# Optimization experiments

Hardware: AMD Instinct MI355X
Metric: run time of the kernel (lower is better)

## Reference

```python
import jax, jax.numpy as jnp
import numpy as np

B_CAPS, C_CAPS, KSZ, STRIDE, N_ITER = 32, 32, 3, 2, 3


def setup_inputs() -> dict:
    key = jax.random.key(0)
    k1, k2, k3, k4, k5 = jax.random.split(key, 5)
    b, Bc, Cc, Win = 8, B_CAPS, C_CAPS, 13
    pose = 0.5 * jax.random.normal(k1, (b, 16 * Bc, Win, Win), jnp.float32)
    act = 0.05 + 0.9 * jax.random.uniform(k2, (b, Bc, Win, Win), jnp.float32)
    x = jnp.concatenate([pose, act], axis=1)
    W = 0.3 * jax.random.normal(k3, (KSZ, KSZ, Bc, Cc, 4, 4), jnp.float32)
    beta_v = jax.random.normal(k4, (1,), jnp.float32)
    beta_a = jax.random.normal(k5, (1,), jnp.float32)
    lambda_ = jnp.ones((1,), jnp.float32)
    return {"x": x, "W": W, "beta_v": beta_v, "beta_a": beta_a, "lambda_": lambda_}


def _conv_caps(x, W, beta_v, beta_a, lambda_):
    B, C, K, s, n_iter = B_CAPS, C_CAPS, KSZ, STRIDE, N_ITER
    b, Win = x.shape[0], x.shape[2]
    Wout = (Win - K) // s + 1
    # channel layout of pose is (4,4,B) row-major, per the original .view(-1,4,4,B,...)
    pose = x[:, :-B].reshape(b, 4, 4, B, Win, Win)
    act = x[:, -B:]
    ks = jnp.arange(K)
    Iidx = s * jnp.arange(Wout)[None, :] + ks[:, None]  # (K,Wout): i_in = s*x + ki
    Ir = Iidx[:, None, :, None]  # (K,1,Wout,1)
    Ic = Iidx[None, :, None, :]  # (1,K,1,Wout)
    # pose patches: (b,4,4,B,K,K,Wout,Wout); matrix dims are (q=rows, r=cols)
    pp = pose[:, :, :, :, Ir, Ic]
    # votes[n,o,ki,kj,x,y,c,p,r] = sum_q W[ki,kj,o,c,p,q] * pose[n,q,r,o,ki,kj,x,y]
    votes = jnp.einsum('ijocpq,nqroijxy->noijxycpr', W, pp)
    votes = votes.reshape(b, B, K, K, Wout, Wout, C, 16)
    a_patch = act[:, :, Ir, Ic]  # (b,B,K,K,Wout,Wout)
    # original E-step indexes votes at pos = stride*x - i, which is <=0 and wraps
    # (torch negative indexing) to (-ki) % K.  Faithfully reproduce that permutation.
    kperm = (-ks) % K
    votesE = votes[:, :, kperm][:, :, :, kperm]
    # routing weights kept in patch form R[i_in=s*x+ki, j_in=s*y+kj, x, y] -> (ki,kj,x,y);
    # this is exactly the set of R entries the original ever reads or writes.
    Rp = jnp.full((b, B, K, K, Wout, Wout, C), 1.0 / (Wout * Wout * C), x.dtype)
    TWO_PI = np.float32(2.0 * np.pi)
    lam = jnp.reshape(lambda_, ())
    mu = act_out = None
    for it in range(n_iter):
        # ---- M-step ----
        r_hat = Rp * a_patch[..., None]                      # (b,B,K,K,Wo,Wo,C)
        sum_r = r_hat.sum(axis=(1, 2, 3))                    # (b,Wo,Wo,C)
        mu = jnp.einsum('noijxyc,noijxycd->nxycd', r_hat, votes) / sum_r[..., None]
        mu_b = mu[:, None, None, None]                       # (b,1,1,1,Wo,Wo,C,16)
        sigma = jnp.einsum('noijxyc,noijxycd->nxycd', r_hat, (votes - mu_b) ** 2) / sum_r[..., None]
        cost = (beta_v + jnp.log(sigma)) * sum_r[..., None]  # (b,Wo,Wo,C,16)
        act_out = jax.nn.sigmoid(lam * (beta_a - cost.sum(-1)))  # (b,Wo,Wo,C)
        # ---- E-step (skipped on last iter: its R is never read afterwards) ----
        if it < n_iter - 1:
            # original: p = exp(-(V-mu)^2)/sqrt(2*pi*sigma), prod over 16 pose dims
            p = jnp.prod(jnp.exp(-(votesE - mu_b) ** 2) / jnp.sqrt(TWO_PI * sigma[:, None, None, None]), axis=-1)
            p_hat = act_out[:, None, None, None] * p         # (b,B,K,K,Wo,Wo,C)
            T = p_hat.sum(-1)                                # (b,B,K,K,Wo,Wo)
            # normalizer is per (batch, input-type, input-position): scatter-add over
            # all (ki,x),(kj,y) mapping to the same input pixel, summed over C
            D = jnp.zeros((b, B, Win, Win), x.dtype).at[:, :, Ir, Ic].add(T)
            Rp = p_hat / D[:, :, Ir, Ic][..., None]
    mus = mu.transpose(0, 3, 4, 1, 2).reshape(b, C * 16, Wout, Wout)
    acts = act_out.transpose(0, 3, 1, 2)                     # (b,C,Wo,Wo)
    return jnp.concatenate([mus, acts], axis=1)              # (b, C*17, Wo, Wo)


def reference(x, W, beta_v, beta_a, lambda_):
    return _conv_caps(x, W, beta_v, beta_a, lambda_)
```

## Files before the change

kernel.cpp:

```cpp
#include <hip/hip_runtime.h>


typedef float v2f __attribute__((ext_vector_type(2)));
typedef float v4f __attribute__((ext_vector_type(4)));

#define OFF_PHAT 0
#define OFF_D0   2654208
#define OFF_D1   2697472
#define OFF_POST 2740736
#define OFF_ACTT 3432960
#define OFF_WT2  3476224

__device__ __forceinline__ float wred64(float v) {
#pragma unroll
  for (int m = 32; m >= 1; m >>= 1) v += __shfl_xor(v, m, 64);
  return v;
}

__device__ __forceinline__ v2f lo2(v4f a) { return __builtin_shufflevector(a, a, 0, 1); }
__device__ __forceinline__ v2f hi2(v4f a) { return __builtin_shufflevector(a, a, 2, 3); }

__global__ __launch_bounds__(256) void prep_kernel(
    const float* __restrict__ x, const float* __restrict__ Wt,
    float* __restrict__ posT, float* __restrict__ actT,
    float* __restrict__ Wt2, float* __restrict__ Dz) {
  int tid = blockIdx.x * 256 + threadIdx.x;
  if (tid < 692224) {
    int pix = tid % 169; int t = tid / 169;
    int o = t & 31; t >>= 5;
    int d = t & 15; int n = t >> 4;
    float v = x[((size_t)n * 544 + d * 32 + o) * 169 + pix];
    posT[((size_t)(n * 32 + o) * 169 + pix) * 16 + d] = v;
  } else if (tid < 735488) {
    int r = tid - 692224;
    int pix = r % 169; int t = r / 169;
    int o = t & 31; int n = t >> 5;
    float v = x[(size_t)n * 91936 + 86528 + o * 169 + pix];
    actT[((size_t)n * 169 + pix) * 32 + o] = v;
  } else if (tid < 882944) {
    int r = tid - 735488;
    int c = r / 4608; int s = r - c * 4608;
    int ch = s >> 4, d = s & 15;
    Wt2[r] = Wt[(size_t)ch * 512 + c * 16 + d];
  } else {
    Dz[tid - 882944] = 0.f;
  }
}

__global__ __launch_bounds__(256, 4) void em_kernel(
    const float* __restrict__ Wt2, const float* __restrict__ posT,
    const float* __restrict__ actT, float* __restrict__ p_hat,
    const float* __restrict__ Dread, float* __restrict__ Dwrite,
    const float* __restrict__ beta_v, const float* __restrict__ beta_a,
    const float* __restrict__ lambda_, float* __restrict__ out, int mode) {
  __shared__ float sP[288 * 20];
  __shared__ float sE[288];
  __shared__ float sPh[4 * 288];

  const int g = blockIdx.x & 7;
  const int sg = blockIdx.x >> 3;
  const int wave = threadIdx.x >> 6;
  const int lane = threadIdx.x & 63;
  const int c = g * 4 + wave;

  int t = sg;
  const int y = t % 6; t /= 6;
  const int xx = t % 6;
  const int n = t / 6;

  const float bvv = beta_v[0], bav = beta_a[0], lamv = lambda_[0];
  const float* wbase = Wt2 + (size_t)c * 4608;

  float phv[5];
  if (mode != 0) {
    const float* phb = p_hat + ((size_t)sg * 32 + c) * 288;
#pragma unroll
    for (int k = 0; k < 5; ++k) {
      int ch = lane + 64 * k; if (ch > 287) ch = 287;
      phv[k] = phb[ch];
    }
  }

  for (int task = threadIdx.x; task < 1152; task += 256) {
    int ch = task >> 2, q = task & 3;
    int o = ch & 31, ij = ch >> 5;
    int i = ij / 3, j = ij - i * 3;
    int pix = (2 * xx + i) * 13 + (2 * y + j);
    v4f v = *(const v4f*)(posT +
        ((size_t)((n * 32 + o) * 169) + pix) * 16 + q * 4);
    *(v4f*)(sP + ch * 20 + q * 4) = v;
  }
  for (int task = threadIdx.x; task < 288; task += 256) {
    int o = task & 31, ij = task >> 5;
    int i = ij / 3, j = ij - i * 3;
    int idx = ((size_t)n * 169 + (2 * xx + i) * 13 + (2 * y + j)) * 32 + o;
    float a = actT[idx];
    sE[task] = (mode == 0) ? a * (1.0f / 1152.0f) : a / Dread[idx];
  }
  __syncthreads();

  float sum_r = 0.f;
  v2f sv2[8], sq2[8];
#pragma unroll
  for (int d = 0; d < 8; ++d) { sv2[d] = 0.f; sq2[d] = 0.f; }

#pragma unroll
  for (int k = 0; k < 5; ++k) {
    int ch = lane + 64 * k;
    const bool act_l = (ch < 288);
    const int chm = act_l ? ch : 0;

    const v4f* Pp = (const v4f*)(sP + chm * 20);
    v4f P0 = Pp[0], P1 = Pp[1], P2 = Pp[2], P3 = Pp[3];
    const v4f* Wp = (const v4f*)(wbase + chm * 16);
    v4f W0 = Wp[0], W1 = Wp[1], W2 = Wp[2], W3 = Wp[3];

    float rhat = sE[chm];
    if (mode != 0) rhat *= phv[k];
    if (!act_l) rhat = 0.f;
    sum_r += rhat;

    v2f PL0 = lo2(P0), PH0 = hi2(P0), PL1 = lo2(P1), PH1 = hi2(P1);
    v2f PL2 = lo2(P2), PH2 = hi2(P2), PL3 = lo2(P3), PH3 = hi2(P3);
    v2f r2 = rhat;

#pragma unroll
    for (int p = 0; p < 4; ++p) {
      v4f Wr = (p == 0) ? W0 : (p == 1) ? W1 : (p == 2) ? W2 : W3;
      v2f vlo = Wr.x * PL0 + Wr.y * PL1 + Wr.z * PL2 + Wr.w * PL3;
      v2f vhi = Wr.x * PH0 + Wr.y * PH1 + Wr.z * PH2 + Wr.w * PH3;
      v2f tlo = r2 * vlo, thi = r2 * vhi;
      sv2[p * 2 + 0] += tlo;
      sv2[p * 2 + 1] += thi;
      sq2[p * 2 + 0] += tlo * vlo;
      sq2[p * 2 + 1] += thi * vhi;
    }
  }

  sum_r = wred64(sum_r);
  const float inv_sr = 1.0f / sum_r;
  float mu[16];
  float lsum = 0.f;
#pragma unroll
  for (int d = 0; d < 16; ++d) {
    float s1 = wred64(sv2[d >> 1][d & 1]);
    float s2 = wred64(sq2[d >> 1][d & 1]);
    float m = s1 * inv_sr;
    mu[d] = m;
    float sg_ = fmaxf(s2 * inv_sr - m * m, 1e-30f);
    lsum += __logf(sg_);
  }
  const float cost = (16.f * bvv + lsum) * sum_r;
  const float aout = 1.0f / (1.0f + __expf(-lamv * (bav - cost)));

  if (mode == 2) {
    if (lane == 0) {
      float* ob = out + (size_t)(n * 544 + c * 16) * 36 + xx * 6 + y;
#pragma unroll
      for (int d = 0; d < 16; ++d) ob[d * 36] = mu[d];
      out[(size_t)(n * 544 + 512 + c) * 36 + xx * 6 + y] = aout;
    }
    return;
  }

  v2f mu2[8];
#pragma unroll
  for (int d = 0; d < 8; ++d) { mu2[d].x = mu[2 * d]; mu2[d].y = mu[2 * d + 1]; }
  const float G = __logf(aout) - 0.5f * (lsum + 16.f * 1.8378770664093453f);

#pragma unroll
  for (int k = 0; k < 5; ++k) {
    int mch = lane + 64 * k;
    if (mch < 288) {
      const v4f* Pp = (const v4f*)(sP + mch * 20);
      v4f P0 = Pp[0], P1 = Pp[1], P2 = Pp[2], P3 = Pp[3];
      const v4f* Wp = (const v4f*)(wbase + mch * 16);
      v4f W0 = Wp[0], W1 = Wp[1], W2 = Wp[2], W3 = Wp[3];

      v2f PL0 = lo2(P0), PH0 = hi2(P0), PL1 = lo2(P1), PH1 = hi2(P1);
      v2f PL2 = lo2(P2), PH2 = hi2(P2), PL3 = lo2(P3), PH3 = hi2(P3);
      v2f ss2 = 0.f;
#pragma unroll
      for (int p = 0; p < 4; ++p) {
        v4f Wr = (p == 0) ? W0 : (p == 1) ? W1 : (p == 2) ? W2 : W3;
        v2f vlo = Wr.x * PL0 + Wr.y * PL1 + Wr.z * PL2 + Wr.w * PL3;
        v2f vhi = Wr.x * PH0 + Wr.y * PH1 + Wr.z * PH2 + Wr.w * PH3;
        v2f dlo = vlo - mu2[p * 2 + 0];
        v2f dhi = vhi - mu2[p * 2 + 1];
        ss2 += dlo * dlo;
        ss2 += dhi * dhi;
      }
      float ss = ss2.x + ss2.y;
      float ph = __expf(G - ss);
      int o = mch & 31, ijm = mch >> 5;
      int im = ijm / 3, jm = ijm - im * 3;
      int i2 = (im == 0) ? 0 : 3 - im;
      int j2 = (jm == 0) ? 0 : 3 - jm;
      int slot = (i2 * 3 + j2) * 32 + o;
      p_hat[((size_t)sg * 32 + c) * 288 + slot] = ph;
      sPh[wave * 288 + slot] = ph;
    }
  }
  __syncthreads();
  for (int t2 = threadIdx.x; t2 < 288; t2 += 256) {
    float s = sPh[t2] + sPh[288 + t2] + sPh[576 + t2] + sPh[864 + t2];
    int o = t2 & 31, ij = t2 >> 5;
    int i = ij / 3, j = ij - i * 3;
    atomicAdd(Dwrite + ((size_t)n * 169 + (2 * xx + i) * 13 + (2 * y + j)) * 32 + o, s);
  }
}

extern "C" void kernel_launch(void* const* d_in, const int* in_sizes, int n_in,
                              void* d_out, int out_size, void* d_ws,
                              size_t ws_size, hipStream_t stream) {
  const float* x   = (const float*)d_in[0];
  const float* Wt  = (const float*)d_in[1];
  const float* bv  = (const float*)d_in[2];
  const float* ba  = (const float*)d_in[3];
  const float* lam = (const float*)d_in[4];
  float* out = (float*)d_out;
  float* ws = (float*)d_ws;

  float* p_hat = ws + OFF_PHAT;
  float* D0    = ws + OFF_D0;
  float* D1    = ws + OFF_D1;
  float* posT  = ws + OFF_POST;
  float* actT  = ws + OFF_ACTT;
  float* Wt2   = ws + OFF_WT2;

  (void)in_sizes; (void)n_in; (void)out_size; (void)ws_size;

  prep_kernel<<<3787, 256, 0, stream>>>(x, Wt, posT, actT, Wt2, D0);

  em_kernel<<<2304, 256, 0, stream>>>(Wt2, posT, actT, p_hat, D1, D0,
                                      bv, ba, lam, out, 0);
  em_kernel<<<2304, 256, 0, stream>>>(Wt2, posT, actT, p_hat, D0, D1,
                                      bv, ba, lam, out, 1);
  em_kernel<<<2304, 256, 0, stream>>>(Wt2, posT, actT, p_hat, D1, D0,
                                      bv, ba, lam, out, 2);
}
```

Before: 169.6 us.

## Stream pose patches through small shared buffer with pixel-major pose layout

Pose data is transposed to a (n,pix,o,d) layout so each pixel's 32 capsules are contiguous. The em kernel now stages two kernel positions at a time into a much smaller shared buffer inside the 5-step loop, instead of loading all 288 rows up front. It also reorders the E-step so each lane writes its permuted slot directly, and spreads the D atomics across loop steps. This cuts LDS use to raise occupancy, in exchange for extra barriers inside the loops and reloading pose data in the second pass.

```diff
diff --git a/kernel.cpp b/kernel.cpp
--- a/kernel.cpp
+++ b/kernel.cpp
@@ -22,7 +22,7 @@
 
 __global__ __launch_bounds__(256) void prep_kernel(
     const float* __restrict__ x, const float* __restrict__ Wt,
-    float* __restrict__ posT, float* __restrict__ actT,
+    float* __restrict__ posT2, float* __restrict__ actT,
     float* __restrict__ Wt2, float* __restrict__ Dz) {
   int tid = blockIdx.x * 256 + threadIdx.x;
   if (tid < 692224) {
@@ -30,7 +30,7 @@
     int o = t & 31; t >>= 5;
     int d = t & 15; int n = t >> 4;
     float v = x[((size_t)n * 544 + d * 32 + o) * 169 + pix];
-    posT[((size_t)(n * 32 + o) * 169 + pix) * 16 + d] = v;
+    posT2[(((size_t)n * 169 + pix) * 32 + o) * 16 + d] = v;
   } else if (tid < 735488) {
     int r = tid - 692224;
     int pix = r % 169; int t = r / 169;
@@ -48,20 +48,21 @@
 }
 
 __global__ __launch_bounds__(256, 4) void em_kernel(
-    const float* __restrict__ Wt2, const float* __restrict__ posT,
+    const float* __restrict__ Wt2, const float* __restrict__ posT2,
     const float* __restrict__ actT, float* __restrict__ p_hat,
     const float* __restrict__ Dread, float* __restrict__ Dwrite,
     const float* __restrict__ beta_v, const float* __restrict__ beta_a,
     const float* __restrict__ lambda_, float* __restrict__ out, int mode) {
-  __shared__ float sP[288 * 20];
-  __shared__ float sE[288];
-  __shared__ float sPh[4 * 288];
+  __shared__ float sPs[2 * 32 * 20];
+  __shared__ float sPh[4 * 64];
 
   const int g = blockIdx.x & 7;
   const int sg = blockIdx.x >> 3;
   const int wave = threadIdx.x >> 6;
   const int lane = threadIdx.x & 63;
   const int c = g * 4 + wave;
+  const int o = lane & 31;
+  const int half = lane >> 5;
 
   int t = sg;
   const int y = t % 6; t /= 6;
@@ -70,34 +71,26 @@
 
   const float bvv = beta_v[0], bav = beta_a[0], lamv = lambda_[0];
   const float* wbase = Wt2 + (size_t)c * 4608;
-
-  float phv[5];
-  if (mode != 0) {
-    const float* phb = p_hat + ((size_t)sg * 32 + c) * 288;
-#pragma unroll
-    for (int k = 0; k < 5; ++k) {
-      int ch = lane + 64 * k; if (ch > 287) ch = 287;
-      phv[k] = phb[ch];
-    }
-  }
-
-  for (int task = threadIdx.x; task < 1152; task += 256) {
-    int ch = task >> 2, q = task & 3;
-    int o = ch & 31, ij = ch >> 5;
-    int i = ij / 3, j = ij - i * 3;
-    int pix = (2 * xx + i) * 13 + (2 * y + j);
-    v4f v = *(const v4f*)(posT +
-        ((size_t)((n * 32 + o) * 169) + pix) * 16 + q * 4);
-    *(v4f*)(sP + ch * 20 + q * 4) = v;
-  }
-  for (int task = threadIdx.x; task < 288; task += 256) {
-    int o = task & 31, ij = task >> 5;
-    int i = ij / 3, j = ij - i * 3;
-    int idx = ((size_t)n * 169 + (2 * xx + i) * 13 + (2 * y + j)) * 32 + o;
+  const float* phb = p_hat + ((size_t)sg * 32 + c) * 288;
+
+  float rh[5];
+#pragma unroll
+  for (int k = 0; k < 5; ++k) {
+    const int ij = half + 2 * k;
+    const bool valid = (ij < 9);
+    const int ijc = valid ? ij : 0;
+    const int i = ijc / 3, j = ijc - 3 * i;
+    const int idx = ((n * 169 + (2 * xx + i) * 13 + (2 * y + j)) * 32) + o;
     float a = actT[idx];
-    sE[task] = (mode == 0) ? a * (1.0f / 1152.0f) : a / Dread[idx];
-  }
-  __syncthreads();
+    float r;
+    if (mode == 0) {
+      r = a * (1.0f / 1152.0f);
+    } else {
+      float ph = phb[valid ? (lane + 64 * k) : 0];
+      r = ph * a * __builtin_amdgcn_rcpf(Dread[idx]);
+    }
+    rh[k] = valid ? r : 0.f;
+  }
 
   float sum_r = 0.f;
   v2f sv2[8], sq2[8];
@@ -106,18 +99,31 @@
 
 #pragma unroll
   for (int k = 0; k < 5; ++k) {
-    int ch = lane + 64 * k;
-    const bool act_l = (ch < 288);
-    const int chm = act_l ? ch : 0;
-
-    const v4f* Pp = (const v4f*)(sP + chm * 20);
+    __syncthreads();
+    {
+      const int tt = threadIdx.x;
+      const int s = tt >> 7, o2 = (tt >> 2) & 31, q = tt & 3;
+      const int ij = 2 * k + s;
+      if (ij < 9) {
+        const int i = ij / 3, j = ij - 3 * i;
+        const int pix = (2 * xx + i) * 13 + (2 * y + j);
+        v4f v = *(const v4f*)(posT2 +
+            ((size_t)((n * 169 + pix) * 32 + o2)) * 16 + q * 4);
+        *(v4f*)(sPs + (s * 32 + o2) * 20 + q * 4) = v;
+      }
+    }
+    __syncthreads();
+
+    const bool valid = (half + 2 * k) < 9;
+    const int row = valid ? lane : 0;
+    const int chm = valid ? (lane + 64 * k) : 0;
+
+    const v4f* Pp = (const v4f*)(sPs + row * 20);
     v4f P0 = Pp[0], P1 = Pp[1], P2 = Pp[2], P3 = Pp[3];
     const v4f* Wp = (const v4f*)(wbase + chm * 16);
     v4f W0 = Wp[0], W1 = Wp[1], W2 = Wp[2], W3 = Wp[3];
 
-    float rhat = sE[chm];
-    if (mode != 0) rhat *= phv[k];
-    if (!act_l) rhat = 0.f;
+    const float rhat = rh[k];
     sum_r += rhat;
 
     v2f PL0 = lo2(P0), PH0 = hi2(P0), PL1 = lo2(P1), PH1 = hi2(P1);
@@ -163,18 +169,45 @@
     return;
   }
 
-  v2f mu2[8];
-#pragma unroll
-  for (int d = 0; d < 8; ++d) { mu2[d].x = mu[2 * d]; mu2[d].y = mu[2 * d + 1]; }
+  v2f nmu2[8];
+#pragma unroll
+  for (int d = 0; d < 8; ++d) { nmu2[d].x = -mu[2 * d]; nmu2[d].y = -mu[2 * d + 1]; }
   const float G = __logf(aout) - 0.5f * (lsum + 16.f * 1.8378770664093453f);
 
 #pragma unroll
   for (int k = 0; k < 5; ++k) {
-    int mch = lane + 64 * k;
-    if (mch < 288) {
-      const v4f* Pp = (const v4f*)(sP + mch * 20);
+    __syncthreads();
+    {
+      const int tt = threadIdx.x;
+      const int s = tt >> 7, o2 = (tt >> 2) & 31, q = tt & 3;
+      const int ij = 2 * k + s;
+      if (ij < 9) {
+        const int i = ij / 3, j = ij - 3 * i;
+        const int i2 = (i == 0) ? 0 : 3 - i;
+        const int j2 = (j == 0) ? 0 : 3 - j;
+        const int pix = (2 * xx + i2) * 13 + (2 * y + j2);
+        v4f v = *(const v4f*)(posT2 +
+            ((size_t)((n * 169 + pix) * 32 + o2)) * 16 + q * 4);
+        *(v4f*)(sPs + (s * 32 + o2) * 20 + q * 4) = v;
+      }
+      if (k > 0 && tt < 64) {
+        const int slotd = 2 * (k - 1) + (tt >> 5), od = tt & 31;
+        float sm = sPh[tt] + sPh[64 + tt] + sPh[128 + tt] + sPh[192 + tt];
+        const int i = slotd / 3, j = slotd - 3 * i;
+        atomicAdd(Dwrite + ((size_t)n * 169 + (2 * xx + i) * 13 + (2 * y + j)) * 32 + od, sm);
+      }
+    }
+    __syncthreads();
+
+    const int ijm = 2 * k + half;
+    float ph = 0.f;
+    if (ijm < 9) {
+      const v4f* Pp = (const v4f*)(sPs + lane * 20);
       v4f P0 = Pp[0], P1 = Pp[1], P2 = Pp[2], P3 = Pp[3];
-      const v4f* Wp = (const v4f*)(wbase + mch * 16);
+      const int i = ijm / 3, j = ijm - 3 * i;
+      const int i2 = (i == 0) ? 0 : 3 - i;
+      const int j2 = (j == 0) ? 0 : 3 - j;
+      const v4f* Wp = (const v4f*)(wbase + ((i2 * 3 + j2) * 32 + o) * 16);
       v4f W0 = Wp[0], W1 = Wp[1], W2 = Wp[2], W3 = Wp[3];
 
       v2f PL0 = lo2(P0), PH0 = hi2(P0), PL1 = lo2(P1), PH1 = hi2(P1);
@@ -185,28 +218,22 @@
         v4f Wr = (p == 0) ? W0 : (p == 1) ? W1 : (p == 2) ? W2 : W3;
         v2f vlo = Wr.x * PL0 + Wr.y * PL1 + Wr.z * PL2 + Wr.w * PL3;
         v2f vhi = Wr.x * PH0 + Wr.y * PH1 + Wr.z * PH2 + Wr.w * PH3;
-        v2f dlo = vlo - mu2[p * 2 + 0];
-        v2f dhi = vhi - mu2[p * 2 + 1];
+        v2f dlo = vlo + nmu2[p * 2 + 0];
+        v2f dhi = vhi + nmu2[p * 2 + 1];
         ss2 += dlo * dlo;
         ss2 += dhi * dhi;
       }
       float ss = ss2.x + ss2.y;
-      float ph = __expf(G - ss);
-      int o = mch & 31, ijm = mch >> 5;
-      int im = ijm / 3, jm = ijm - im * 3;
-      int i2 = (im == 0) ? 0 : 3 - im;
-      int j2 = (jm == 0) ? 0 : 3 - jm;
-      int slot = (i2 * 3 + j2) * 32 + o;
-      p_hat[((size_t)sg * 32 + c) * 288 + slot] = ph;
-      sPh[wave * 288 + slot] = ph;
-    }
+      ph = __expf(G - ss);
+      p_hat[((size_t)sg * 32 + c) * 288 + ijm * 32 + o] = ph;
+    }
+    sPh[wave * 64 + lane] = ph;
   }
   __syncthreads();
-  for (int t2 = threadIdx.x; t2 < 288; t2 += 256) {
-    float s = sPh[t2] + sPh[288 + t2] + sPh[576 + t2] + sPh[864 + t2];
-    int o = t2 & 31, ij = t2 >> 5;
-    int i = ij / 3, j = ij - i * 3;
-    atomicAdd(Dwrite + ((size_t)n * 169 + (2 * xx + i) * 13 + (2 * y + j)) * 32 + o, s);
+  if (threadIdx.x < 32) {
+    const int tt = threadIdx.x;
+    float sm = sPh[tt] + sPh[64 + tt] + sPh[128 + tt] + sPh[192 + tt];
+    atomicAdd(Dwrite + ((size_t)n * 169 + (2 * xx + 2) * 13 + (2 * y + 2)) * 32 + tt, sm);
   }
 }
 
@@ -224,18 +251,18 @@
   float* p_hat = ws + OFF_PHAT;
   float* D0    = ws + OFF_D0;
   float* D1    = ws + OFF_D1;
-  float* posT  = ws + OFF_POST;
+  float* posT2 = ws + OFF_POST;
   float* actT  = ws + OFF_ACTT;
   float* Wt2   = ws + OFF_WT2;
 
   (void)in_sizes; (void)n_in; (void)out_size; (void)ws_size;
 
-  prep_kernel<<<3787, 256, 0, stream>>>(x, Wt, posT, actT, Wt2, D0);
-
-  em_kernel<<<2304, 256, 0, stream>>>(Wt2, posT, actT, p_hat, D1, D0,
+  prep_kernel<<<3787, 256, 0, stream>>>(x, Wt, posT2, actT, Wt2, D0);
+
+  em_kernel<<<2304, 256, 0, stream>>>(Wt2, posT2, actT, p_hat, D1, D0,
                                       bv, ba, lam, out, 0);
-  em_kernel<<<2304, 256, 0, stream>>>(Wt2, posT, actT, p_hat, D0, D1,
+  em_kernel<<<2304, 256, 0, stream>>>(Wt2, posT2, actT, p_hat, D0, D1,
                                       bv, ba, lam, out, 1);
-  em_kernel<<<2304, 256, 0, stream>>>(Wt2, posT, actT, p_hat, D1, D0,
+  em_kernel<<<2304, 256, 0, stream>>>(Wt2, posT2, actT, p_hat, D1, D0,
                                       bv, ba, lam, out, 2);
 }
```

New measurement: 260.9 us. 1.54x slower.
